# Optimization experiments

Measured on AMD Instinct MI355X. Metric: run time of the kernel, lower is better.

## Reference

```python
import jax, jax.numpy as jnp
import numpy as np

K = 12  # nsample_k; graph per point has K nodes (self + K-1 abs-diff neighbors)


def setup_inputs() -> dict:
    key = jax.random.key(0)
    k1, k2, k3 = jax.random.split(key, 3)
    p = jax.random.normal(k1, (2, 8192, 3), dtype=jnp.float32)
    W = jax.random.normal(k2, (1, 3), dtype=jnp.float32) * 0.5  # GCNConv lin weight [out=1, in=3]
    b = jax.random.normal(k3, (1,), dtype=jnp.float32) * 0.1    # GCNConv bias
    return {"p": p, "W": W, "b": b}


def _knn_idx(pts, k):
    # k nearest neighbors over the whole flattened cloud, self included then dropped
    pts = jax.lax.stop_gradient(pts)  # indices are non-differentiable
    sq = jnp.sum(pts * pts, axis=-1)                      # [n]
    d2 = sq[:, None] + sq[None, :] - 2.0 * (pts @ pts.T)  # [n, n] squared distances
    _, idx = jax.lax.top_k(-d2, k)                        # ascending distance
    return idx[:, 1:]                                     # drop self -> [n, k-1]


def reference(p, W, b):
    # p: [B, N, 3] -> flatten to [n, 3]
    pts = p.reshape(-1, 3)
    nidx = _knn_idx(pts, K)            # [n, K-1]
    nbr = pts[nidx]                    # [n, K-1, 3]
    # node features of each star graph: node 0 = point, nodes 1..K-1 = |p - neighbor|
    p_ij = jnp.concatenate([pts[:, None, :], jnp.abs(pts[:, None, :] - nbr)], axis=1)  # [n, K, 3]
    # GCNConv(3,1) on identical star graphs (edges 0->j, plus self loops), closed form:
    #   deg0 = 1, deg_j = 2  =>  out0 = x0 W^T + b ; out_j = x0 W^T / sqrt(2) + x_j W^T / 2 + b
    xw = jnp.einsum('nkc,oc->nko', p_ij, W)  # [n, K, 1]
    inv_s2 = 1.0 / jnp.sqrt(jnp.float32(2.0))
    out0 = xw[:, :1] + b                                  # [n, 1, 1]
    outj = inv_s2 * xw[:, :1] + 0.5 * xw[:, 1:] + b       # [n, K-1, 1]
    emb = jnp.concatenate([out0, outj], axis=1)           # [n, K, 1]
    # POOL: squeeze -> [n, K]; AdaptiveAvgPool1d(1) -> [n, 1]; module returns avg only
    return jnp.mean(emb[..., 0], axis=1, keepdims=True)   # [n, 1]
```

## Files before the change

kernel.cpp:

```cpp
#include <hip/hip_runtime.h>
#include <math.h>


#define NBINS  2048
#define PARTS  16
#define CMIN_  (-6.0f)
#define INVBW_ ((float)NBINS / 12.0f)
#define BLOCK  256
#define WPB    4
#define SEED   768
#define KK     12
#define CD     4
#define BIG    3.0e38f

__device__ __forceinline__ int bin_of(float x) {
  int b = (int)((x - CMIN_) * INVBW_);
  b = b < 0 ? 0 : b;
  b = b > NBINS - 1 ? NBINS - 1 : b;
  return b;
}

__device__ __forceinline__ float wave_min(float v) {
#pragma unroll
  for (int o = 1; o < 64; o <<= 1) v = fminf(v, __shfl_xor(v, o));
  return v;
}

__device__ __forceinline__ void ins4(float (&qd)[CD], float (&qw)[CD],
                                     float d, float w) {
#pragma unroll
  for (int k = CD - 1; k >= 1; --k) {
    const bool up  = (qd[k - 1] > d);
    const bool mid = (qd[k] > d);
    const float nd = up ? qd[k - 1] : (mid ? d : qd[k]);
    const float nw = up ? qw[k - 1] : (mid ? w : qw[k]);
    qd[k] = nd; qw[k] = nw;
  }
  if (qd[0] > d) { qw[0] = w; qd[0] = d; }
}

__global__ __launch_bounds__(1024)
void sort_kernel(const float* __restrict__ p, int* __restrict__ c_all,
                 float4* __restrict__ s_all, int n) {
  __shared__ int h_all[NBINS];
  __shared__ int h_pre[NBINS];
  __shared__ int wsum[16];
  const int tid  = threadIdx.x;
  const int dim  = blockIdx.x / PARTS;
  const int part = blockIdx.x % PARTS;
  const int chunk   = (n + PARTS - 1) / PARTS;
  const int myStart = part * chunk;
  const int myEnd   = min(myStart + chunk, n);

  h_all[tid] = 0; h_all[tid + 1024] = 0;
  h_pre[tid] = 0; h_pre[tid + 1024] = 0;
  __syncthreads();

  for (int i = tid; i < n; i += 1024) {
    const int b = bin_of(p[3 * i + dim]);
    atomicAdd(&h_all[b], 1);
    if (i < myStart) atomicAdd(&h_pre[b], 1);
  }
  __syncthreads();

  const int a = h_all[2 * tid], b = h_all[2 * tid + 1];
  const int v = a + b;
  const int lane = tid & 63, wid = tid >> 6;
  int incl = v;
#pragma unroll
  for (int o = 1; o < 64; o <<= 1) {
    const int t = __shfl_up(incl, o);
    if (lane >= o) incl += t;
  }
  if (lane == 63) wsum[wid] = incl;
  __syncthreads();
  int woff = 0;
  for (int wI = 0; wI < wid; ++wI) woff += wsum[wI];
  const int excl = woff + incl - v;

  if (part == 0) {
    int* __restrict__ cursor = c_all + (size_t)dim * NBINS;
    cursor[2 * tid]     = excl + a;
    cursor[2 * tid + 1] = excl + a + b;
  }

  const int c0 = excl + h_pre[2 * tid];
  const int c1 = excl + a + h_pre[2 * tid + 1];
  __syncthreads();
  h_pre[2 * tid]     = c0;
  h_pre[2 * tid + 1] = c1;
  __syncthreads();

  float4* __restrict__ sorted = s_all + (size_t)dim * n;
  for (int i = myStart + tid; i < myEnd; i += 1024) {
    const float x = p[3 * i], y = p[3 * i + 1], z = p[3 * i + 2];
    const float c = (dim == 0) ? x : (dim == 1) ? y : z;
    const int pos = atomicAdd(&h_pre[bin_of(c)], 1);
    sorted[pos] = make_float4(x, y, z, __int_as_float(i));
  }
}

__global__ __launch_bounds__(BLOCK)
void query_kernel(const float4* __restrict__ sx, const float4* __restrict__ sy,
                  const float4* __restrict__ sz, const int* __restrict__ cx,
                  const int* __restrict__ cy, const int* __restrict__ cz,
                  const float* __restrict__ W, const float* __restrict__ bias,
                  float* __restrict__ out, int n) {
  const int lane = threadIdx.x & 63;
  const int wv   = threadIdx.x >> 6;
  const int t    = wv * (n >> 2) + blockIdx.x;
  const float W0 = W[0], W1 = W[1], W2 = W[2];
  const float bb = bias[0];

  const float4 me = sx[t];
  const float xi = me.x, yi = me.y, zi = me.z;
  const int orig = __float_as_int(me.w);

  const float ax = fabsf(xi), ay = fabsf(yi), az = fabsf(zi);
  const float4* sv; const int* cur; float cq;
  if (ay >= ax && ay >= az)      { sv = sy; cur = cy; cq = yi; }
  else if (az >= ax && az >= ay) { sv = sz; cur = cz; cq = zi; }
  else                           { sv = sx; cur = cx; cq = xi; }

  const int bq = bin_of(cq);
  const int bs = (bq > 0) ? cur[bq - 1] : 0;
  const int be = cur[bq];
  int lo = ((bs + be) >> 1) - SEED / 2;
  lo = lo < 0 ? 0 : lo;
  lo = lo > n - SEED ? n - SEED : lo;
  const float4* base = sv + lo + lane;

  float m = BIG;
#pragma unroll
  for (int s = 0; s < SEED / 64; ++s) {
    const float4 c = base[s * 64];
    const float dx = xi - c.x, dy = yi - c.y, dz = zi - c.z;
    m = fminf(m, fmaf(dx, dx, fmaf(dy, dy, dz * dz)));
  }

  float u;
  {
    float v = m;
#pragma unroll
    for (int r = 0; r < KK; ++r) {
      const float mm = wave_min(v);
      u = mm;
      v = (v == mm) ? BIG : v;
    }
  }

  const float s = sqrtf(u);
  const int bl = bin_of(cq - s);
  const int bh = bin_of(cq + s);
  const int lo2 = (bl > 0) ? cur[bl - 1] : 0;
  const int hi2 = cur[bh];
  const int steps = (hi2 - lo2 + 63) >> 6;

  float qd[CD], qw[CD];
  int ccnt = 0;
#pragma unroll
  for (int k = 0; k < CD; ++k) { qd[k] = BIG; qw[k] = 0.f; }

  int st = 0;
  for (; st + 2 <= steps; st += 2) {
    const int p0 = lo2 + st * 64 + lane;
    const int p1 = p0 + 64;
    const float4 c0 = sv[p0];
    const float4 c1 = sv[(p1 < hi2) ? p1 : hi2 - 1];
    {
      const float dx = xi - c0.x, dy = yi - c0.y, dz = zi - c0.z;
      const float d2 = fmaf(dx, dx, fmaf(dy, dy, dz * dz));
      if (d2 <= u) {
        const float w = fmaf(W0, fabsf(dx), fmaf(W1, fabsf(dy), W2 * fabsf(dz)));
        ++ccnt; ins4(qd, qw, d2, w);
      }
    }
    if (p1 < hi2) {
      const float dx = xi - c1.x, dy = yi - c1.y, dz = zi - c1.z;
      const float d2 = fmaf(dx, dx, fmaf(dy, dy, dz * dz));
      if (d2 <= u) {
        const float w = fmaf(W0, fabsf(dx), fmaf(W1, fabsf(dy), W2 * fabsf(dz)));
        ++ccnt; ins4(qd, qw, d2, w);
      }
    }
  }
  for (; st < steps; ++st) {
    const int pos = lo2 + st * 64 + lane;
    if (pos < hi2) {
      const float4 c = sv[pos];
      const float dx = xi - c.x, dy = yi - c.y, dz = zi - c.z;
      const float d2 = fmaf(dx, dx, fmaf(dy, dy, dz * dz));
      if (d2 <= u) {
        const float w = fmaf(W0, fabsf(dx), fmaf(W1, fabsf(dy), W2 * fabsf(dz)));
        ++ccnt; ins4(qd, qw, d2, w);
      }
    }
  }

  float acc = 0.f;
  const bool ovf = __ballot(ccnt > CD) != 0ULL;
  if (!ovf) {
#pragma unroll
    for (int r = 0; r < KK; ++r) {
      const float mm = wave_min(qd[0]);
      const unsigned long long bal = __ballot(qd[0] == mm);
      if (qd[0] == mm && lane == (int)(__ffsll(bal) - 1)) {
        acc += qw[0];
#pragma unroll
        for (int k = 0; k < CD - 1; ++k) { qd[k] = qd[k + 1]; qw[k] = qw[k + 1]; }
        qd[CD - 1] = BIG;
      }
    }
  } else {
    float dd[KK];
#pragma unroll
    for (int k = 0; k < KK; ++k) dd[k] = BIG;
    for (int s0 = 0; s0 < steps; ++s0) {
      const int pos = lo2 + s0 * 64 + lane;
      const float4 c = sv[(pos < hi2) ? pos : hi2 - 1];
      const float dx = xi - c.x, dy = yi - c.y, dz = zi - c.z;
      const float d2 = (pos < hi2) ? fmaf(dx, dx, fmaf(dy, dy, dz * dz)) : BIG;
#pragma unroll
      for (int k = KK - 1; k >= 1; --k)
        dd[k] = __builtin_amdgcn_fmed3f(d2, dd[k - 1], dd[k]);
      dd[0] = fminf(dd[0], d2);
    }
    float tau = 0.f;
#pragma unroll
    for (int r = 0; r < KK; ++r) {
      const float mm = wave_min(dd[0]);
      if (dd[0] == mm) {
#pragma unroll
        for (int k = 0; k < KK - 1; ++k) dd[k] = dd[k + 1];
        dd[KK - 1] = BIG;
      }
      tau = mm;
    }
    for (int s0 = 0; s0 < steps; ++s0) {
      const int pos = lo2 + s0 * 64 + lane;
      if (pos < hi2) {
        const float4 c = sv[pos];
        const float dx = xi - c.x, dy = yi - c.y, dz = zi - c.z;
        const float d2 = fmaf(dx, dx, fmaf(dy, dy, dz * dz));
        const float w  = fmaf(W0, fabsf(dx), fmaf(W1, fabsf(dy), W2 * fabsf(dz)));
        acc += (d2 <= tau) ? w : 0.f;
      }
    }
  }

#pragma unroll
  for (int o = 1; o < 64; o <<= 1) acc += __shfl_xor(acc, o);
  if (lane == 0) {
    const float xw0 = W0 * xi + W1 * yi + W2 * zi;
    out[orig] = bb + (xw0 * 8.778174593052022f + 0.5f * acc) * (1.0f / 12.0f);
  }
}

extern "C" void kernel_launch(void* const* d_in, const int* in_sizes, int n_in,
                              void* d_out, int out_size, void* d_ws, size_t ws_size,
                              hipStream_t stream) {
  const float* p  = (const float*)d_in[0];
  const float* W  = (const float*)d_in[1];
  const float* bb = (const float*)d_in[2];
  float* out = (float*)d_out;

  const int n = in_sizes[0] / 3;

  int*    c_all = (int*)d_ws;
  float4* s_all = (float4*)((char*)d_ws + 3 * NBINS * 4);
  int*    cx = c_all;
  int*    cy = cx + NBINS;
  int*    cz = cy + NBINS;
  float4* sx = s_all;
  float4* sy = sx + n;
  float4* sz = sy + n;

  sort_kernel<<<3 * PARTS, 1024, 0, stream>>>(p, c_all, s_all, n);
  query_kernel<<<n / WPB, BLOCK, 0, stream>>>(sx, sy, sz, cx, cy, cz, W, bb, out, n);
}
```

Before: 121.4 us.

## Process two query points per wavefront with interleaved search loops

Each wavefront now handles two consecutive sorted query points (A and B) instead of one. The seed scan, wave-min reductions, candidate scan and top-12 extraction are interleaved so independent loads and shuffles from both queries can overlap, hiding latency and halving the number of waves. The query-to-wave mapping also changes from strided (wave*n/4+block) to contiguous, which changes memory locality. The cost is higher register pressure, and the two queries can diverge in step count or overflow fallback, leaving part of the wave idle.

```diff
diff --git a/kernel.cpp b/kernel.cpp
--- a/kernel.cpp
+++ b/kernel.cpp
@@ -7,7 +7,6 @@
 #define CMIN_  (-6.0f)
 #define INVBW_ ((float)NBINS / 12.0f)
 #define BLOCK  256
-#define WPB    4
 #define SEED   768
 #define KK     12
 #define CD     4
@@ -100,6 +99,107 @@
   }
 }
 
+struct Q {
+  float xi, yi, zi, cq;
+  int orig;
+  const float4* sv;
+  const int* cur;
+};
+
+__device__ __forceinline__ Q make_q(const float4* sx, const float4* sy,
+                                    const float4* sz, const int* cx,
+                                    const int* cy, const int* cz, int t) {
+  Q q;
+  const float4 me = sx[t];
+  q.xi = me.x; q.yi = me.y; q.zi = me.z; q.orig = __float_as_int(me.w);
+  const float ax = fabsf(q.xi), ay = fabsf(q.yi), az = fabsf(q.zi);
+  if (ay >= ax && ay >= az)      { q.sv = sy; q.cur = cy; q.cq = q.yi; }
+  else if (az >= ax && az >= ay) { q.sv = sz; q.cur = cz; q.cq = q.zi; }
+  else                           { q.sv = sx; q.cur = cx; q.cq = q.xi; }
+  return q;
+}
+
+__device__ __forceinline__ int seed_lo(const Q& q, int n) {
+  const int bq = bin_of(q.cq);
+  const int bs = (bq > 0) ? q.cur[bq - 1] : 0;
+  const int be = q.cur[bq];
+  int lo = ((bs + be) >> 1) - SEED / 2;
+  lo = lo < 0 ? 0 : lo;
+  lo = lo > n - SEED ? n - SEED : lo;
+  return lo;
+}
+
+__device__ __forceinline__ float extract12(float (&qd)[CD], float (&qw)[CD],
+                                           int lane) {
+  float acc = 0.f;
+#pragma unroll
+  for (int r = 0; r < KK; ++r) {
+    const float mm = wave_min(qd[0]);
+    const unsigned long long bal = __ballot(qd[0] == mm);
+    if (qd[0] == mm && lane == (int)(__ffsll(bal) - 1)) {
+      acc += qw[0];
+#pragma unroll
+      for (int k = 0; k < CD - 1; ++k) { qd[k] = qd[k + 1]; qw[k] = qw[k + 1]; }
+      qd[CD - 1] = BIG;
+    }
+  }
+  return acc;
+}
+
+__device__ __forceinline__ float fallback12(const Q& q, int lo2, int hi2,
+                                            int steps, float W0, float W1,
+                                            float W2, int lane) {
+  float dd[KK];
+#pragma unroll
+  for (int k = 0; k < KK; ++k) dd[k] = BIG;
+  for (int s0 = 0; s0 < steps; ++s0) {
+    const int pos = lo2 + s0 * 64 + lane;
+    const float4 c = q.sv[(pos < hi2) ? pos : hi2 - 1];
+    const float dx = q.xi - c.x, dy = q.yi - c.y, dz = q.zi - c.z;
+    const float d2 = (pos < hi2) ? fmaf(dx, dx, fmaf(dy, dy, dz * dz)) : BIG;
+#pragma unroll
+    for (int k = KK - 1; k >= 1; --k)
+      dd[k] = __builtin_amdgcn_fmed3f(d2, dd[k - 1], dd[k]);
+    dd[0] = fminf(dd[0], d2);
+  }
+  float tau = 0.f;
+#pragma unroll
+  for (int r = 0; r < KK; ++r) {
+    const float mm = wave_min(dd[0]);
+    if (dd[0] == mm) {
+#pragma unroll
+      for (int k = 0; k < KK - 1; ++k) dd[k] = dd[k + 1];
+      dd[KK - 1] = BIG;
+    }
+    tau = mm;
+  }
+  float acc = 0.f;
+  for (int s0 = 0; s0 < steps; ++s0) {
+    const int pos = lo2 + s0 * 64 + lane;
+    if (pos < hi2) {
+      const float4 c = q.sv[pos];
+      const float dx = q.xi - c.x, dy = q.yi - c.y, dz = q.zi - c.z;
+      const float d2 = fmaf(dx, dx, fmaf(dy, dy, dz * dz));
+      const float w  = fmaf(W0, fabsf(dx), fmaf(W1, fabsf(dy), W2 * fabsf(dz)));
+      acc += (d2 <= tau) ? w : 0.f;
+    }
+  }
+  return acc;
+}
+
+__device__ __forceinline__ void step1(const Q& q, float u, int pos, int hi2,
+                                      float W0, float W1, float W2,
+                                      float (&qd)[CD], float (&qw)[CD],
+                                      int& ccnt) {
+  const float4 c = q.sv[(pos < hi2) ? pos : hi2 - 1];
+  const float dx = q.xi - c.x, dy = q.yi - c.y, dz = q.zi - c.z;
+  const float d2 = fmaf(dx, dx, fmaf(dy, dy, dz * dz));
+  if (d2 <= u && pos < hi2) {
+    const float w = fmaf(W0, fabsf(dx), fmaf(W1, fabsf(dy), W2 * fabsf(dz)));
+    ++ccnt; ins4(qd, qw, d2, w);
+  }
+}
+
 __global__ __launch_bounds__(BLOCK)
 void query_kernel(const float4* __restrict__ sx, const float4* __restrict__ sy,
                   const float4* __restrict__ sz, const int* __restrict__ cx,
@@ -108,151 +208,126 @@
                   float* __restrict__ out, int n) {
   const int lane = threadIdx.x & 63;
   const int wv   = threadIdx.x >> 6;
-  const int t    = wv * (n >> 2) + blockIdx.x;
+  const int gw   = blockIdx.x * (BLOCK / 64) + wv;
   const float W0 = W[0], W1 = W[1], W2 = W[2];
   const float bb = bias[0];
 
-  const float4 me = sx[t];
-  const float xi = me.x, yi = me.y, zi = me.z;
-  const int orig = __float_as_int(me.w);
-
-  const float ax = fabsf(xi), ay = fabsf(yi), az = fabsf(zi);
-  const float4* sv; const int* cur; float cq;
-  if (ay >= ax && ay >= az)      { sv = sy; cur = cy; cq = yi; }
-  else if (az >= ax && az >= ay) { sv = sz; cur = cz; cq = zi; }
-  else                           { sv = sx; cur = cx; cq = xi; }
-
-  const int bq = bin_of(cq);
-  const int bs = (bq > 0) ? cur[bq - 1] : 0;
-  const int be = cur[bq];
-  int lo = ((bs + be) >> 1) - SEED / 2;
-  lo = lo < 0 ? 0 : lo;
-  lo = lo > n - SEED ? n - SEED : lo;
-  const float4* base = sv + lo + lane;
-
-  float m = BIG;
+  Q a = make_q(sx, sy, sz, cx, cy, cz, 2 * gw);
+  Q b = make_q(sx, sy, sz, cx, cy, cz, 2 * gw + 1);
+
+  const float4* baseA = a.sv + seed_lo(a, n) + lane;
+  const float4* baseB = b.sv + seed_lo(b, n) + lane;
+
+  float mA = BIG, mB = BIG;
 #pragma unroll
   for (int s = 0; s < SEED / 64; ++s) {
-    const float4 c = base[s * 64];
-    const float dx = xi - c.x, dy = yi - c.y, dz = zi - c.z;
-    m = fminf(m, fmaf(dx, dx, fmaf(dy, dy, dz * dz)));
-  }
-
-  float u;
+    const float4 cA = baseA[s * 64];
+    const float4 cB = baseB[s * 64];
+    {
+      const float dx = a.xi - cA.x, dy = a.yi - cA.y, dz = a.zi - cA.z;
+      mA = fminf(mA, fmaf(dx, dx, fmaf(dy, dy, dz * dz)));
+    }
+    {
+      const float dx = b.xi - cB.x, dy = b.yi - cB.y, dz = b.zi - cB.z;
+      mB = fminf(mB, fmaf(dx, dx, fmaf(dy, dy, dz * dz)));
+    }
+  }
+
+  float uA, uB;
   {
-    float v = m;
+    float vA = mA, vB = mB;
 #pragma unroll
     for (int r = 0; r < KK; ++r) {
-      const float mm = wave_min(v);
-      u = mm;
-      v = (v == mm) ? BIG : v;
-    }
-  }
-
-  const float s = sqrtf(u);
-  const int bl = bin_of(cq - s);
-  const int bh = bin_of(cq + s);
-  const int lo2 = (bl > 0) ? cur[bl - 1] : 0;
-  const int hi2 = cur[bh];
-  const int steps = (hi2 - lo2 + 63) >> 6;
-
-  float qd[CD], qw[CD];
-  int ccnt = 0;
-#pragma unroll
-  for (int k = 0; k < CD; ++k) { qd[k] = BIG; qw[k] = 0.f; }
+      float wA = vA, wB = vB;
+#pragma unroll
+      for (int o = 1; o < 64; o <<= 1) {
+        wA = fminf(wA, __shfl_xor(wA, o));
+        wB = fminf(wB, __shfl_xor(wB, o));
+      }
+      uA = wA; uB = wB;
+      vA = (vA == wA) ? BIG : vA;
+      vB = (vB == wB) ? BIG : vB;
+    }
+  }
+
+  int lo2A, hi2A, lo2B, hi2B;
+  {
+    const float sA = sqrtf(uA);
+    const int blA = bin_of(a.cq - sA), bhA = bin_of(a.cq + sA);
+    lo2A = (blA > 0) ? a.cur[blA - 1] : 0;
+    hi2A = a.cur[bhA];
+    const float sB = sqrtf(uB);
+    const int blB = bin_of(b.cq - sB), bhB = bin_of(b.cq + sB);
+    lo2B = (blB > 0) ? b.cur[blB - 1] : 0;
+    hi2B = b.cur[bhB];
+  }
+  const int stepsA = (hi2A - lo2A + 63) >> 6;
+  const int stepsB = (hi2B - lo2B + 63) >> 6;
+  const int stepsMin = min(stepsA, stepsB);
+
+  float qdA[CD], qwA[CD], qdB[CD], qwB[CD];
+  int ccA = 0, ccB = 0;
+#pragma unroll
+  for (int k = 0; k < CD; ++k) {
+    qdA[k] = BIG; qwA[k] = 0.f; qdB[k] = BIG; qwB[k] = 0.f;
+  }
 
   int st = 0;
-  for (; st + 2 <= steps; st += 2) {
-    const int p0 = lo2 + st * 64 + lane;
-    const int p1 = p0 + 64;
-    const float4 c0 = sv[p0];
-    const float4 c1 = sv[(p1 < hi2) ? p1 : hi2 - 1];
-    {
-      const float dx = xi - c0.x, dy = yi - c0.y, dz = zi - c0.z;
-      const float d2 = fmaf(dx, dx, fmaf(dy, dy, dz * dz));
-      if (d2 <= u) {
-        const float w = fmaf(W0, fabsf(dx), fmaf(W1, fabsf(dy), W2 * fabsf(dz)));
-        ++ccnt; ins4(qd, qw, d2, w);
+  for (; st < stepsMin; ++st) {
+    const int posA = lo2A + st * 64 + lane;
+    const int posB = lo2B + st * 64 + lane;
+    step1(a, uA, posA, hi2A, W0, W1, W2, qdA, qwA, ccA);
+    step1(b, uB, posB, hi2B, W0, W1, W2, qdB, qwB, ccB);
+  }
+  for (; st < stepsA; ++st)
+    step1(a, uA, lo2A + st * 64 + lane, hi2A, W0, W1, W2, qdA, qwA, ccA);
+  for (; st < stepsB; ++st)
+    step1(b, uB, lo2B + st * 64 + lane, hi2B, W0, W1, W2, qdB, qwB, ccB);
+
+  float accA = 0.f, accB = 0.f;
+  const bool ovfA = __ballot(ccA > CD) != 0ULL;
+  const bool ovfB = __ballot(ccB > CD) != 0ULL;
+  if (!ovfA && !ovfB) {
+#pragma unroll
+    for (int r = 0; r < KK; ++r) {
+      float ma = qdA[0], mb = qdB[0];
+#pragma unroll
+      for (int o = 1; o < 64; o <<= 1) {
+        ma = fminf(ma, __shfl_xor(ma, o));
+        mb = fminf(mb, __shfl_xor(mb, o));
       }
-    }
-    if (p1 < hi2) {
-      const float dx = xi - c1.x, dy = yi - c1.y, dz = zi - c1.z;
-      const float d2 = fmaf(dx, dx, fmaf(dy, dy, dz * dz));
-      if (d2 <= u) {
-        const float w = fmaf(W0, fabsf(dx), fmaf(W1, fabsf(dy), W2 * fabsf(dz)));
-        ++ccnt; ins4(qd, qw, d2, w);
+      const unsigned long long balA = __ballot(qdA[0] == ma);
+      const unsigned long long balB = __ballot(qdB[0] == mb);
+      if (qdA[0] == ma && lane == (int)(__ffsll(balA) - 1)) {
+        accA += qwA[0];
+#pragma unroll
+        for (int k = 0; k < CD - 1; ++k) { qdA[k] = qdA[k + 1]; qwA[k] = qwA[k + 1]; }
+        qdA[CD - 1] = BIG;
       }
-    }
-  }
-  for (; st < steps; ++st) {
-    const int pos = lo2 + st * 64 + lane;
-    if (pos < hi2) {
-      const float4 c = sv[pos];
-      const float dx = xi - c.x, dy = yi - c.y, dz = zi - c.z;
-      const float d2 = fmaf(dx, dx, fmaf(dy, dy, dz * dz));
-      if (d2 <= u) {
-        const float w = fmaf(W0, fabsf(dx), fmaf(W1, fabsf(dy), W2 * fabsf(dz)));
-        ++ccnt; ins4(qd, qw, d2, w);
+      if (qdB[0] == mb && lane == (int)(__ffsll(balB) - 1)) {
+        accB += qwB[0];
+#pragma unroll
+        for (int k = 0; k < CD - 1; ++k) { qdB[k] = qdB[k + 1]; qwB[k] = qwB[k + 1]; }
+        qdB[CD - 1] = BIG;
       }
     }
-  }
-
-  float acc = 0.f;
-  const bool ovf = __ballot(ccnt > CD) != 0ULL;
-  if (!ovf) {
-#pragma unroll
-    for (int r = 0; r < KK; ++r) {
-      const float mm = wave_min(qd[0]);
-      const unsigned long long bal = __ballot(qd[0] == mm);
-      if (qd[0] == mm && lane == (int)(__ffsll(bal) - 1)) {
-        acc += qw[0];
-#pragma unroll
-        for (int k = 0; k < CD - 1; ++k) { qd[k] = qd[k + 1]; qw[k] = qw[k + 1]; }
-        qd[CD - 1] = BIG;
-      }
-    }
   } else {
-    float dd[KK];
-#pragma unroll
-    for (int k = 0; k < KK; ++k) dd[k] = BIG;
-    for (int s0 = 0; s0 < steps; ++s0) {
-      const int pos = lo2 + s0 * 64 + lane;
-      const float4 c = sv[(pos < hi2) ? pos : hi2 - 1];
-      const float dx = xi - c.x, dy = yi - c.y, dz = zi - c.z;
-      const float d2 = (pos < hi2) ? fmaf(dx, dx, fmaf(dy, dy, dz * dz)) : BIG;
-#pragma unroll
-      for (int k = KK - 1; k >= 1; --k)
-        dd[k] = __builtin_amdgcn_fmed3f(d2, dd[k - 1], dd[k]);
-      dd[0] = fminf(dd[0], d2);
-    }
-    float tau = 0.f;
-#pragma unroll
-    for (int r = 0; r < KK; ++r) {
-      const float mm = wave_min(dd[0]);
-      if (dd[0] == mm) {
-#pragma unroll
-        for (int k = 0; k < KK - 1; ++k) dd[k] = dd[k + 1];
-        dd[KK - 1] = BIG;
-      }
-      tau = mm;
-    }
-    for (int s0 = 0; s0 < steps; ++s0) {
-      const int pos = lo2 + s0 * 64 + lane;
-      if (pos < hi2) {
-        const float4 c = sv[pos];
-        const float dx = xi - c.x, dy = yi - c.y, dz = zi - c.z;
-        const float d2 = fmaf(dx, dx, fmaf(dy, dy, dz * dz));
-        const float w  = fmaf(W0, fabsf(dx), fmaf(W1, fabsf(dy), W2 * fabsf(dz)));
-        acc += (d2 <= tau) ? w : 0.f;
-      }
-    }
-  }
-
-#pragma unroll
-  for (int o = 1; o < 64; o <<= 1) acc += __shfl_xor(acc, o);
+    accA = ovfA ? fallback12(a, lo2A, hi2A, stepsA, W0, W1, W2, lane)
+                : extract12(qdA, qwA, lane);
+    accB = ovfB ? fallback12(b, lo2B, hi2B, stepsB, W0, W1, W2, lane)
+                : extract12(qdB, qwB, lane);
+  }
+
+#pragma unroll
+  for (int o = 1; o < 64; o <<= 1) {
+    accA += __shfl_xor(accA, o);
+    accB += __shfl_xor(accB, o);
+  }
   if (lane == 0) {
-    const float xw0 = W0 * xi + W1 * yi + W2 * zi;
-    out[orig] = bb + (xw0 * 8.778174593052022f + 0.5f * acc) * (1.0f / 12.0f);
+    const float xwA = W0 * a.xi + W1 * a.yi + W2 * a.zi;
+    const float xwB = W0 * b.xi + W1 * b.yi + W2 * b.zi;
+    out[a.orig] = bb + (xwA * 8.778174593052022f + 0.5f * accA) * (1.0f / 12.0f);
+    out[b.orig] = bb + (xwB * 8.778174593052022f + 0.5f * accB) * (1.0f / 12.0f);
   }
 }
 
@@ -276,5 +351,5 @@
   float4* sz = sy + n;
 
   sort_kernel<<<3 * PARTS, 1024, 0, stream>>>(p, c_all, s_all, n);
-  query_kernel<<<n / WPB, BLOCK, 0, stream>>>(sx, sy, sz, cx, cy, cz, W, bb, out, n);
-}
+  query_kernel<<<n / 8, BLOCK, 0, stream>>>(sx, sy, sz, cx, cy, cz, W, bb, out, n);
+}
```

Measured after the change: 129.6 us. 1.07x slower.
